# Performance work log

Measured on AMD Instinct MI355X. Metric: run time of the kernel, lower is better.

The kernel has to match this reference:

```python
import jax, jax.numpy as jnp
import numpy as np

B, S, D, H = 4, 2048, 1024, 16
HD = D // H


def setup_inputs() -> dict:
    key = jax.random.key(0)
    ks = jax.random.split(key, 11)
    s = 1.0 / np.sqrt(D)
    return {
        "query": jax.random.normal(ks[0], (B, S, D), jnp.float32),
        "key": jax.random.normal(ks[1], (B, S, D), jnp.float32),
        "value": jax.random.normal(ks[2], (B, S, D), jnp.float32),
        "Wq": jax.random.normal(ks[3], (D, D), jnp.float32) * s,
        "bq": jax.random.normal(ks[4], (D,), jnp.float32) * s,
        "Wk": jax.random.normal(ks[5], (D, D), jnp.float32) * s,
        "bk": jax.random.normal(ks[6], (D,), jnp.float32) * s,
        "Wv": jax.random.normal(ks[7], (D, D), jnp.float32) * s,
        "bv": jax.random.normal(ks[8], (D,), jnp.float32) * s,
        "Wo": jax.random.normal(ks[9], (D, D), jnp.float32) * s,
        "bo": jax.random.normal(ks[10], (D,), jnp.float32) * s,
    }


def reference(query, key, value, Wq, bq, Wk, bk, Wv, bv, Wo, bo):
    b = query.shape[0]
    # projections (torch Linear: x @ W.T + b)
    q = (query @ Wq.T + bq).reshape(b, -1, H, HD).transpose(0, 2, 1, 3)  # [B,H,S,hd]
    k = (key @ Wk.T + bk).reshape(b, -1, H, HD).transpose(0, 2, 1, 3)
    v = (value @ Wv.T + bv).reshape(b, -1, H, HD).transpose(0, 2, 1, 3)
    scores = jnp.einsum('bhqd,bhkd->bhqk', q, k) / jnp.sqrt(jnp.float32(HD))
    attn = jax.nn.softmax(scores, axis=-1)  # dropout = identity (eval)
    out = jnp.einsum('bhqk,bhkd->bhqd', attn, v)
    out = out.transpose(0, 2, 1, 3).reshape(b, -1, D)
    return out @ Wo.T + bo
```

## Files before the change

### kernel.cpp

```cpp
#include <hip/hip_runtime.h>
#include <stdint.h>

typedef __attribute__((ext_vector_type(8))) short  s16x8;
typedef __attribute__((ext_vector_type(4))) float  f32x4;
typedef __attribute__((ext_vector_type(4))) unsigned short u16x4;

__device__ __forceinline__ unsigned short f2bf(float f) {
  union { float f; uint32_t u; } x; x.f = f;
  uint32_t u = x.u;
  return (unsigned short)((u + 0x7fffu + ((u >> 16) & 1u)) >> 16);
}

__device__ __forceinline__ float fexp2(float x) {
  float r; asm("v_exp_f32 %0, %1" : "=v"(r) : "v"(x)); return r;
}
__device__ __forceinline__ uint32_t cvtpk_bf16(float lo, float hi) {
  uint32_t r; asm("v_cvt_pk_bf16_f32 %0, %1, %2" : "=v"(r) : "v"(lo), "v"(hi)); return r;
}

__device__ __forceinline__ void gload_lds16(const void* g, void* l) {
  __builtin_amdgcn_global_load_lds(
      (const __attribute__((address_space(1))) void*)g,
      (__attribute__((address_space(3))) void*)l, 16, 0, 0);
}

struct CvtJobs {
  const float* src[7];
  unsigned short* dst[7];
  int n4[7];
};
__global__ __launch_bounds__(256) void cvt_all(CvtJobs jobs) {
  const int j = blockIdx.y;
  const float* __restrict__ src = jobs.src[j];
  unsigned short* __restrict__ dst = jobs.dst[j];
  const int n4 = jobs.n4[j];
  const int stride = gridDim.x * blockDim.x;
  for (int i = blockIdx.x * blockDim.x + threadIdx.x; i < n4; i += stride) {
    f32x4 v = *(const f32x4*)(src + (size_t)i * 4);
    u16x4 o = { f2bf(v[0]), f2bf(v[1]), f2bf(v[2]), f2bf(v[3]) };
    *(u16x4*)(dst + (size_t)i * 4) = o;
  }
}

struct GemmJob {
  const unsigned short* A;
  const unsigned short* Bmat;
  const float* bias;
  unsigned short* C;
  int M, N, Nb;
  int bias_row;
  float scale;
};

__device__ __forceinline__ void gemm_core8big(const unsigned short* __restrict__ A,
                                              const unsigned short* __restrict__ Bw,
                                              int m0, int n0, int K, char* L,
                                              f32x4 (&acc)[8][4]) {
  const int tid = threadIdx.x;
  const int l = tid & 63;
  const int lr = l & 15, lc = l >> 4;
  const int w = tid >> 6;
  const int wr = w >> 2, wc = w & 3;

  const int srow = tid >> 2;
  const int sc = (tid & 3) ^ ((srow >> 1) & 3);
  const unsigned short* sA1 = A + (size_t)(m0 + srow) * K + sc * 8;
  const unsigned short* sA2 = sA1 + (size_t)128 * K;
  const unsigned short* sB1 = Bw + (size_t)(n0 + srow) * K + sc * 8;
  const unsigned short* sB2 = sB1 + (size_t)128 * K;
  char* d1 = L + (size_t)tid * 16;
  char* d2 = d1 + 8192;
  char* d3 = d1 + 16384;
  char* d4 = d1 + 24576;

#define GSTAGE(BUF, KS) { gload_lds16(sA1 + (KS), d1 + (BUF) * 32768); \
                          gload_lds16(sA2 + (KS), d2 + (BUF) * 32768); \
                          gload_lds16(sB1 + (KS), d3 + (BUF) * 32768); \
                          gload_lds16(sB2 + (KS), d4 + (BUF) * 32768); }

  const int s16 = (lc ^ ((lr >> 1) & 3)) * 16;
  int offA[8], offB[4];
#pragma unroll
  for (int i = 0; i < 8; ++i) offA[i] = (wr * 128 + i * 16 + lr) * 64 + s16;
#pragma unroll
  for (int j = 0; j < 4; ++j) offB[j] = 16384 + (wc * 64 + j * 16 + lr) * 64 + s16;

  const int nk = K >> 5;
  GSTAGE(0, 0);
  GSTAGE(1, 32);
  int cur = 0;
  for (int t = 0; t < nk; ++t) {
    if (t < nk - 1) asm volatile("s_waitcnt vmcnt(4)" ::: "memory");
    else            asm volatile("s_waitcnt vmcnt(0)" ::: "memory");
    __builtin_amdgcn_s_barrier();
    if (t < nk - 2) {
      int nb = cur + 2; if (nb >= 3) nb -= 3;
      GSTAGE(nb, (t + 2) * 32);
    }
    const char* Lb = L + cur * 32768;
    s16x8 af[8], bfr[4];
#pragma unroll
    for (int i = 0; i < 8; ++i) af[i] = *(const s16x8*)(Lb + offA[i]);
#pragma unroll
    for (int j = 0; j < 4; ++j) bfr[j] = *(const s16x8*)(Lb + offB[j]);
    __builtin_amdgcn_s_setprio(1);
#pragma unroll
    for (int i = 0; i < 8; ++i)
#pragma unroll
      for (int j = 0; j < 4; ++j)
        acc[i][j] = __builtin_amdgcn_mfma_f32_16x16x32_bf16(af[i], bfr[j], acc[i][j], 0, 0, 0);
    __builtin_amdgcn_s_setprio(0);
    ++cur; if (cur == 3) cur = 0;
  }
#undef GSTAGE
}

__global__ __launch_bounds__(512) void gemm_qkv(GemmJob j0, GemmJob j1, GemmJob j2) {
  __shared__ __align__(16) char L[98304];
  const int f = blockIdx.x;
  const int wid = (f & 7) * 48 + (f >> 3);
  const int job = wid >> 7;
  const int i = wid & 127;
  const GemmJob jb = (job == 0) ? j0 : (job == 1) ? j1 : j2;
  const int m0 = (i / jb.Nb) * 256, n0 = (i % jb.Nb) * 256;
  f32x4 acc[8][4];
#pragma unroll
  for (int i2 = 0; i2 < 8; ++i2)
#pragma unroll
    for (int j2 = 0; j2 < 4; ++j2) acc[i2][j2] = (f32x4){0.f, 0.f, 0.f, 0.f};
  gemm_core8big(jb.A, jb.Bmat, m0, n0, 1024, L, acc);
  const int tid = threadIdx.x;
  const int l = tid & 63, w = tid >> 6;
  const int lr = l & 15, lc = l >> 4;
  const int wr = w >> 2, wc = w & 3;
#pragma unroll
  for (int i2 = 0; i2 < 8; ++i2) {
    const int row0 = m0 + wr * 128 + i2 * 16 + lc * 4;
    f32x4 brow;
    if (jb.bias_row) brow = *(const f32x4*)&jb.bias[row0];
#pragma unroll
    for (int j2 = 0; j2 < 4; ++j2) {
      const int col = n0 + wc * 64 + j2 * 16 + lr;
      float bcol = jb.bias_row ? 0.f : jb.bias[col];
#pragma unroll
      for (int r = 0; r < 4; ++r) {
        float v = (acc[i2][j2][r] + (jb.bias_row ? brow[r] : bcol)) * jb.scale;
        jb.C[(size_t)(row0 + r) * jb.N + col] = f2bf(v);
      }
    }
  }
}

__global__ __launch_bounds__(512) void gemm_out(const unsigned short* __restrict__ A,
                                                const unsigned short* __restrict__ Bw,
                                                const float* __restrict__ bias,
                                                float* __restrict__ Cout,
                                                int M, int N, int K) {
  __shared__ __align__(16) char L[98304];
  const int f = blockIdx.x;
  const int wid = (f & 7) * 16 + (f >> 3);
  const int m0 = (wid >> 2) * 256, n0 = (wid & 3) * 256;
  f32x4 acc[8][4];
#pragma unroll
  for (int i = 0; i < 8; ++i)
#pragma unroll
    for (int j = 0; j < 4; ++j) acc[i][j] = (f32x4){0.f, 0.f, 0.f, 0.f};
  gemm_core8big(A, Bw, m0, n0, K, L, acc);
  const int tid = threadIdx.x;
  const int l = tid & 63, w = tid >> 6;
  const int lr = l & 15, lc = l >> 4;
  const int wr = w >> 2, wc = w & 3;
#pragma unroll
  for (int i = 0; i < 8; ++i) {
    const int row0 = m0 + wr * 128 + i * 16 + lc * 4;
#pragma unroll
    for (int j = 0; j < 4; ++j) {
      const int col = n0 + wc * 64 + j * 16 + lr;
      float bcol = bias[col];
#pragma unroll
      for (int r = 0; r < 4; ++r)
        Cout[(size_t)(row0 + r) * N + col] = acc[i][j][r] + bcol;
    }
  }
}

__global__ __launch_bounds__(512) void attn_fwd(const unsigned short* __restrict__ qb,
                                                const unsigned short* __restrict__ kb,
                                                const unsigned short* __restrict__ vtb,
                                                unsigned short* __restrict__ ob) {
  __shared__ __align__(16) unsigned short L[3 * 8192];
  const int tid = threadIdx.x;
  const int l = tid & 63, w = tid >> 6;
  const int lr = l & 15, lc = l >> 4;
  const int i0 = blockIdx.x;
  const int wid = (i0 & 7) * 128 + (i0 >> 3);
  const int qx = wid & 15;
  const int h = (wid >> 4) & 15;
  const int b = wid >> 8;
  const int q0 = qx * 128;
  const size_t qkbase = ((size_t)b * 2048) * 1024 + (size_t)h * 64;
  const size_t vtbase = (size_t)(h * 64) * 8192 + (size_t)b * 2048;

  s16x8 aq0, aq1;
  {
    const unsigned short* qp = qb + qkbase + (size_t)(q0 + w * 16 + lr) * 1024 + lc * 8;
    aq0 = *(const s16x8*)qp;
    aq1 = *(const s16x8*)(qp + 32);
  }

  float lsum = 0.f;
  f32x4 oacc[4];
#pragma unroll
  for (int nd = 0; nd < 4; ++nd) oacc[nd] = (f32x4){0.f, 0.f, 0.f, 0.f};

  const int role = w >> 2, wk = w & 3;
  const int rl = l >> 3;
  const int cs = (l & 7) ^ rl;
  const int rA = wk * 16 + rl, rB = rA + 8;
#define RHO(rr) (8 * (((rr) >> 2) & 3) + 4 * (((rr) >> 4) & 1) + ((rr) & 3) + 32 * ((rr) >> 5))
  const unsigned short* sA;
  const unsigned short* sB;
  size_t tstep;
  if (role == 0) {
    sA = kb + qkbase + (size_t)RHO(rA) * 1024 + cs * 8;
    sB = kb + qkbase + (size_t)RHO(rB) * 1024 + cs * 8;
    tstep = (size_t)64 * 1024;
  } else {
    sA = vtb + vtbase + (size_t)rA * 8192 + cs * 8;
    sB = vtb + vtbase + (size_t)rB * 8192 + cs * 8;
    tstep = 64;
  }
#undef RHO
  char* dstL = (char*)L + role * 8192 + wk * 2048 + l * 16;

#define STAGE(BUF, T) {                                              \
    gload_lds16(sA + (size_t)(T) * tstep, dstL + (BUF) * 16384);     \
    gload_lds16(sB + (size_t)(T) * tstep, dstL + (BUF) * 16384 + 1024); }

  int off0[4];
#pragma unroll
  for (int ni = 0; ni < 4; ++ni)
    off0[ni] = (ni * 16 + lr) * 128 + ((lc ^ (lr & 7)) * 16);

  STAGE(0, 0);
  STAGE(1, 1);

  int cur = 0;
  for (int t = 0; t < 32; ++t) {
    if (t < 31) asm volatile("s_waitcnt vmcnt(2)" ::: "memory");
    else        asm volatile("s_waitcnt vmcnt(0)" ::: "memory");
    __builtin_amdgcn_s_barrier();
    if (t < 30) {
      int nb = cur + 2; if (nb >= 3) nb -= 3;
      STAGE(nb, t + 2);
    }
    const char* Lb = (const char*)L + cur * 16384;

    f32x4 sf[4];
    __builtin_amdgcn_s_setprio(1);
#pragma unroll
    for (int ni = 0; ni < 4; ++ni) {
      s16x8 k0 = *(const s16x8*)(Lb + off0[ni]);
      s16x8 k1 = *(const s16x8*)(Lb + (off0[ni] ^ 64));
      f32x4 z = (f32x4){0.f, 0.f, 0.f, 0.f};
      z = __builtin_amdgcn_mfma_f32_16x16x32_bf16(k0, aq0, z, 0, 0, 0);
      z = __builtin_amdgcn_mfma_f32_16x16x32_bf16(k1, aq1, z, 0, 0, 0);
      sf[ni] = z;
    }
    __builtin_amdgcn_s_setprio(0);

    union { uint32_t u[4]; s16x8 v; } pa0u, pa1u;
#pragma unroll
    for (int ni = 0; ni < 4; ++ni) {
      float p0 = fexp2(sf[ni][0]);
      float p1 = fexp2(sf[ni][1]);
      float p2 = fexp2(sf[ni][2]);
      float p3 = fexp2(sf[ni][3]);
      lsum += (p0 + p1) + (p2 + p3);
      uint32_t w0 = cvtpk_bf16(p0, p1);
      uint32_t w1 = cvtpk_bf16(p2, p3);
      if (ni < 2) { pa0u.u[ni * 2] = w0; pa0u.u[ni * 2 + 1] = w1; }
      else        { pa1u.u[(ni - 2) * 2] = w0; pa1u.u[(ni - 2) * 2 + 1] = w1; }
    }

    __builtin_amdgcn_s_setprio(1);
#pragma unroll
    for (int nd = 0; nd < 4; ++nd) {
      s16x8 v0 = *(const s16x8*)(Lb + 8192 + off0[nd]);
      s16x8 v1 = *(const s16x8*)(Lb + 8192 + (off0[nd] ^ 64));
      oacc[nd] = __builtin_amdgcn_mfma_f32_16x16x32_bf16(pa0u.v, v0, oacc[nd], 0, 0, 0);
      oacc[nd] = __builtin_amdgcn_mfma_f32_16x16x32_bf16(pa1u.v, v1, oacc[nd], 0, 0, 0);
    }
    __builtin_amdgcn_s_setprio(0);

    ++cur; if (cur == 3) cur = 0;
  }

  lsum += __shfl_xor(lsum, 16, 64);
  lsum += __shfl_xor(lsum, 32, 64);
  float linv[4];
#pragma unroll
  for (int r = 0; r < 4; ++r) linv[r] = 1.f / __shfl(lsum, lc * 4 + r, 64);
#pragma unroll
  for (int nd = 0; nd < 4; ++nd)
#pragma unroll
    for (int r = 0; r < 4; ++r) {
      int qrow = q0 + w * 16 + lc * 4 + r;
      ob[qkbase + (size_t)qrow * 1024 + nd * 16 + lr] = f2bf(oacc[nd][r] * linv[r]);
    }
#undef STAGE
}

extern "C" void kernel_launch(void* const* d_in, const int* in_sizes, int n_in,
                              void* d_out, int out_size, void* d_ws, size_t ws_size,
                              hipStream_t stream) {
  const float* query = (const float*)d_in[0];
  const float* key_  = (const float*)d_in[1];
  const float* value = (const float*)d_in[2];
  const float* Wq = (const float*)d_in[3];
  const float* bq = (const float*)d_in[4];
  const float* Wk = (const float*)d_in[5];
  const float* bk = (const float*)d_in[6];
  const float* Wv = (const float*)d_in[7];
  const float* bv = (const float*)d_in[8];
  const float* Wo = (const float*)d_in[9];
  const float* bo = (const float*)d_in[10];

  const int MS = 4 * 2048;
  const int D = 1024;
  const size_t NX = (size_t)MS * D;
  const size_t NW = (size_t)D * D;

  const size_t need = (6 * NX + 4 * NW) * 2;
  if (ws_size < need) return;

  unsigned short* ws  = (unsigned short*)d_ws;
  unsigned short* xq  = ws;
  unsigned short* xk  = xq + NX;
  unsigned short* xv  = xk + NX;
  unsigned short* qb_ = xv + NX;
  unsigned short* kb_ = qb_ + NX;
  unsigned short* vtb = kb_ + NX;
  unsigned short* wqb = vtb + NX;
  unsigned short* wkb = wqb + NW;
  unsigned short* wvb = wkb + NW;
  unsigned short* wob = wvb + NW;
  unsigned short* attn = xq;

  CvtJobs cj;
  cj.src[0] = query; cj.dst[0] = xq;  cj.n4[0] = (int)(NX / 4);
  cj.src[1] = key_;  cj.dst[1] = xk;  cj.n4[1] = (int)(NX / 4);
  cj.src[2] = value; cj.dst[2] = xv;  cj.n4[2] = (int)(NX / 4);
  cj.src[3] = Wq;    cj.dst[3] = wqb; cj.n4[3] = (int)(NW / 4);
  cj.src[4] = Wk;    cj.dst[4] = wkb; cj.n4[4] = (int)(NW / 4);
  cj.src[5] = Wv;    cj.dst[5] = wvb; cj.n4[5] = (int)(NW / 4);
  cj.src[6] = Wo;    cj.dst[6] = wob; cj.n4[6] = (int)(NW / 4);
  cvt_all<<<dim3(1024, 7), 256, 0, stream>>>(cj);

  const float qscale = 0.18033688f;
  GemmJob jq = { xq,  wqb, bq, qb_, MS, D,  4,  0, qscale };
  GemmJob jk = { xk,  wkb, bk, kb_, MS, D,  4,  0, 1.f };
  GemmJob jv = { wvb, xv,  bv, vtb, D,  MS, 32, 1, 1.f };
  gemm_qkv<<<dim3(384), 512, 0, stream>>>(jq, jk, jv);

  attn_fwd<<<dim3(1024), 512, 0, stream>>>(qb_, kb_, vtb, attn);

  gemm_out<<<dim3(128), 512, 0, stream>>>(attn, wob, bo, (float*)d_out, MS, D, D);
}
```

Baseline: 214.3 us.

## Restructure GEMM core to K=64 double-buffered stages and compute softmax row sums via MFMA

The shared GEMM core now stages 64-wide K tiles into a two-buffer LDS layout (128KB) with an 8-way XOR swizzle. Each K tile is split into four MFMA phases, with barriers between them and the global-to-LDS loads for the next tiles placed inside the loop. This halves the number of outer iterations and is meant to overlap loading with compute, at the cost of more LDS per block and extra barriers. Separately, the attention kernel drops the per-lane VALU sum of exponentials and the shuffle reduction. It instead gets row sums from an extra pair of MFMAs against a bf16 ones vector, which sums the bf16-rounded probabilities.

```diff
diff --git a/kernel.cpp b/kernel.cpp
--- a/kernel.cpp
+++ b/kernel.cpp
@@ -23,6 +23,8 @@
       (const __attribute__((address_space(1))) void*)g,
       (__attribute__((address_space(3))) void*)l, 16, 0, 0);
 }
+
+#define PBAR() { asm volatile("" ::: "memory"); __builtin_amdgcn_s_barrier(); }
 
 struct CvtJobs {
   const float* src[7];
@@ -52,71 +54,109 @@
   float scale;
 };
 
-__device__ __forceinline__ void gemm_core8big(const unsigned short* __restrict__ A,
-                                              const unsigned short* __restrict__ Bw,
-                                              int m0, int n0, int K, char* L,
-                                              f32x4 (&acc)[8][4]) {
+__device__ __forceinline__ void gemm_core256(const unsigned short* __restrict__ A,
+                                             const unsigned short* __restrict__ Bw,
+                                             int m0, int n0, int K, char* L,
+                                             f32x4 (&acc)[8][4]) {
   const int tid = threadIdx.x;
   const int l = tid & 63;
   const int lr = l & 15, lc = l >> 4;
   const int w = tid >> 6;
   const int wr = w >> 2, wc = w & 3;
 
-  const int srow = tid >> 2;
-  const int sc = (tid & 3) ^ ((srow >> 1) & 3);
-  const unsigned short* sA1 = A + (size_t)(m0 + srow) * K + sc * 8;
-  const unsigned short* sA2 = sA1 + (size_t)128 * K;
-  const unsigned short* sB1 = Bw + (size_t)(n0 + srow) * K + sc * 8;
-  const unsigned short* sB2 = sB1 + (size_t)128 * K;
-  char* d1 = L + (size_t)tid * 16;
-  char* d2 = d1 + 8192;
-  char* d3 = d1 + 16384;
-  char* d4 = d1 + 24576;
-
-#define GSTAGE(BUF, KS) { gload_lds16(sA1 + (KS), d1 + (BUF) * 32768); \
-                          gload_lds16(sA2 + (KS), d2 + (BUF) * 32768); \
-                          gload_lds16(sB1 + (KS), d3 + (BUF) * 32768); \
-                          gload_lds16(sB2 + (KS), d4 + (BUF) * 32768); }
-
-  const int s16 = (lc ^ ((lr >> 1) & 3)) * 16;
+  const int srow = tid >> 3;
+  const int sc = (tid & 7) ^ (srow & 7);
+  const unsigned short* sa0 = A + (size_t)(m0 + srow) * K + sc * 8;
+  const unsigned short* sa1 = A + (size_t)(m0 + 128 + srow) * K + sc * 8;
+  const unsigned short* sb0 = Bw + (size_t)(n0 + srow) * K + sc * 8;
+  const unsigned short* sb1 = Bw + (size_t)(n0 + 128 + srow) * K + sc * 8;
+  const size_t rk64 = (size_t)64 * K;
+  char* dst0 = L + (size_t)tid * 16;
+
+#define STGA(BUF, H, KT) { \
+    const unsigned short* s_ = (H) ? sa1 : sa0; \
+    gload_lds16(s_ + (size_t)(KT) * 64,        dst0 + (BUF) * 65536 + (H) * 16384); \
+    gload_lds16(s_ + rk64 + (size_t)(KT) * 64, dst0 + (BUF) * 65536 + (H) * 16384 + 8192); }
+#define STGB(BUF, H, KT) { \
+    const unsigned short* s_ = (H) ? sb1 : sb0; \
+    gload_lds16(s_ + (size_t)(KT) * 64,        dst0 + (BUF) * 65536 + 32768 + (H) * 16384); \
+    gload_lds16(s_ + rk64 + (size_t)(KT) * 64, dst0 + (BUF) * 65536 + 32768 + (H) * 16384 + 8192); }
+
+  const int c0 = ((lc) ^ (lr & 7)) << 4;
+  const int c1 = ((4 + lc) ^ (lr & 7)) << 4;
   int offA[8], offB[4];
 #pragma unroll
-  for (int i = 0; i < 8; ++i) offA[i] = (wr * 128 + i * 16 + lr) * 64 + s16;
-#pragma unroll
-  for (int j = 0; j < 4; ++j) offB[j] = 16384 + (wc * 64 + j * 16 + lr) * 64 + s16;
-
-  const int nk = K >> 5;
-  GSTAGE(0, 0);
-  GSTAGE(1, 32);
-  int cur = 0;
+  for (int i = 0; i < 8; ++i) offA[i] = (wr * 128 + i * 16 + lr) * 128;
+#pragma unroll
+  for (int j = 0; j < 4; ++j) offB[j] = 32768 + (wc * 64 + j * 16 + lr) * 128;
+
+  const int nk = K >> 6;
+  STGA(0, 0, 0); STGA(0, 1, 0); STGB(0, 0, 0); STGB(0, 1, 0);
+  STGA(1, 0, 1); STGA(1, 1, 1);
+  asm volatile("s_waitcnt vmcnt(4)" ::: "memory");
+  __builtin_amdgcn_s_barrier();
+
   for (int t = 0; t < nk; ++t) {
-    if (t < nk - 1) asm volatile("s_waitcnt vmcnt(4)" ::: "memory");
+    const int buf = t & 1;
+    const char* Lb = L + buf * 65536;
+    s16x8 a0[8], b0[4], a1[8], b1[4];
+
+    if (t + 1 < nk) STGB(buf ^ 1, 0, t + 1);
+#pragma unroll
+    for (int i = 0; i < 8; ++i) a0[i] = *(const s16x8*)(Lb + offA[i] + c0);
+#pragma unroll
+    for (int j = 0; j < 4; ++j) b0[j] = *(const s16x8*)(Lb + offB[j] + c0);
+    __builtin_amdgcn_s_setprio(1);
+#pragma unroll
+    for (int i = 0; i < 8; ++i) {
+      acc[i][0] = __builtin_amdgcn_mfma_f32_16x16x32_bf16(a0[i], b0[0], acc[i][0], 0, 0, 0);
+      acc[i][1] = __builtin_amdgcn_mfma_f32_16x16x32_bf16(a0[i], b0[1], acc[i][1], 0, 0, 0);
+    }
+    __builtin_amdgcn_s_setprio(0);
+    PBAR();
+
+    if (t + 1 < nk) STGB(buf ^ 1, 1, t + 1);
+    __builtin_amdgcn_s_setprio(1);
+#pragma unroll
+    for (int i = 0; i < 8; ++i) {
+      acc[i][2] = __builtin_amdgcn_mfma_f32_16x16x32_bf16(a0[i], b0[2], acc[i][2], 0, 0, 0);
+      acc[i][3] = __builtin_amdgcn_mfma_f32_16x16x32_bf16(a0[i], b0[3], acc[i][3], 0, 0, 0);
+    }
+    __builtin_amdgcn_s_setprio(0);
+    PBAR();
+
+#pragma unroll
+    for (int i = 0; i < 8; ++i) a1[i] = *(const s16x8*)(Lb + offA[i] + c1);
+#pragma unroll
+    for (int j = 0; j < 4; ++j) b1[j] = *(const s16x8*)(Lb + offB[j] + c1);
+    __builtin_amdgcn_s_setprio(1);
+#pragma unroll
+    for (int i = 0; i < 8; ++i) {
+      acc[i][0] = __builtin_amdgcn_mfma_f32_16x16x32_bf16(a1[i], b1[0], acc[i][0], 0, 0, 0);
+      acc[i][1] = __builtin_amdgcn_mfma_f32_16x16x32_bf16(a1[i], b1[1], acc[i][1], 0, 0, 0);
+    }
+    __builtin_amdgcn_s_setprio(0);
+    asm volatile("s_waitcnt lgkmcnt(0)" ::: "memory");
+    __builtin_amdgcn_s_barrier();
+
+    if (t + 2 < nk) { STGA(buf, 0, t + 2); STGA(buf, 1, t + 2); }
+    __builtin_amdgcn_s_setprio(1);
+#pragma unroll
+    for (int i = 0; i < 8; ++i) {
+      acc[i][2] = __builtin_amdgcn_mfma_f32_16x16x32_bf16(a1[i], b1[2], acc[i][2], 0, 0, 0);
+      acc[i][3] = __builtin_amdgcn_mfma_f32_16x16x32_bf16(a1[i], b1[3], acc[i][3], 0, 0, 0);
+    }
+    __builtin_amdgcn_s_setprio(0);
+    if (t + 2 < nk) asm volatile("s_waitcnt vmcnt(4)" ::: "memory");
     else            asm volatile("s_waitcnt vmcnt(0)" ::: "memory");
     __builtin_amdgcn_s_barrier();
-    if (t < nk - 2) {
-      int nb = cur + 2; if (nb >= 3) nb -= 3;
-      GSTAGE(nb, (t + 2) * 32);
-    }
-    const char* Lb = L + cur * 32768;
-    s16x8 af[8], bfr[4];
-#pragma unroll
-    for (int i = 0; i < 8; ++i) af[i] = *(const s16x8*)(Lb + offA[i]);
-#pragma unroll
-    for (int j = 0; j < 4; ++j) bfr[j] = *(const s16x8*)(Lb + offB[j]);
-    __builtin_amdgcn_s_setprio(1);
-#pragma unroll
-    for (int i = 0; i < 8; ++i)
-#pragma unroll
-      for (int j = 0; j < 4; ++j)
-        acc[i][j] = __builtin_amdgcn_mfma_f32_16x16x32_bf16(af[i], bfr[j], acc[i][j], 0, 0, 0);
-    __builtin_amdgcn_s_setprio(0);
-    ++cur; if (cur == 3) cur = 0;
-  }
-#undef GSTAGE
+  }
+#undef STGA
+#undef STGB
 }
 
 __global__ __launch_bounds__(512) void gemm_qkv(GemmJob j0, GemmJob j1, GemmJob j2) {
-  __shared__ __align__(16) char L[98304];
+  __shared__ __align__(16) char L[131072];
   const int f = blockIdx.x;
   const int wid = (f & 7) * 48 + (f >> 3);
   const int job = wid >> 7;
@@ -128,7 +168,7 @@
   for (int i2 = 0; i2 < 8; ++i2)
 #pragma unroll
     for (int j2 = 0; j2 < 4; ++j2) acc[i2][j2] = (f32x4){0.f, 0.f, 0.f, 0.f};
-  gemm_core8big(jb.A, jb.Bmat, m0, n0, 1024, L, acc);
+  gemm_core256(jb.A, jb.Bmat, m0, n0, 1024, L, acc);
   const int tid = threadIdx.x;
   const int l = tid & 63, w = tid >> 6;
   const int lr = l & 15, lc = l >> 4;
@@ -156,7 +196,7 @@
                                                 const float* __restrict__ bias,
                                                 float* __restrict__ Cout,
                                                 int M, int N, int K) {
-  __shared__ __align__(16) char L[98304];
+  __shared__ __align__(16) char L[131072];
   const int f = blockIdx.x;
   const int wid = (f & 7) * 16 + (f >> 3);
   const int m0 = (wid >> 2) * 256, n0 = (wid & 3) * 256;
@@ -165,7 +205,7 @@
   for (int i = 0; i < 8; ++i)
 #pragma unroll
     for (int j = 0; j < 4; ++j) acc[i][j] = (f32x4){0.f, 0.f, 0.f, 0.f};
-  gemm_core8big(A, Bw, m0, n0, K, L, acc);
+  gemm_core256(A, Bw, m0, n0, K, L, acc);
   const int tid = threadIdx.x;
   const int l = tid & 63, w = tid >> 6;
   const int lr = l & 15, lc = l >> 4;
@@ -208,8 +248,13 @@
     aq1 = *(const s16x8*)(qp + 32);
   }
 
-  float lsum = 0.f;
+  union { u16x4 h4[2]; s16x8 v; } onesu;
+#pragma unroll
+  for (int i = 0; i < 2; ++i) onesu.h4[i] = (u16x4){0x3F80, 0x3F80, 0x3F80, 0x3F80};
+  const s16x8 bones = onesu.v;
+
   f32x4 oacc[4];
+  f32x4 oextra = (f32x4){0.f, 0.f, 0.f, 0.f};
 #pragma unroll
   for (int nd = 0; nd < 4; ++nd) oacc[nd] = (f32x4){0.f, 0.f, 0.f, 0.f};
 
@@ -276,7 +321,6 @@
       float p1 = fexp2(sf[ni][1]);
       float p2 = fexp2(sf[ni][2]);
       float p3 = fexp2(sf[ni][3]);
-      lsum += (p0 + p1) + (p2 + p3);
       uint32_t w0 = cvtpk_bf16(p0, p1);
       uint32_t w1 = cvtpk_bf16(p2, p3);
       if (ni < 2) { pa0u.u[ni * 2] = w0; pa0u.u[ni * 2 + 1] = w1; }
@@ -291,16 +335,16 @@
       oacc[nd] = __builtin_amdgcn_mfma_f32_16x16x32_bf16(pa0u.v, v0, oacc[nd], 0, 0, 0);
       oacc[nd] = __builtin_amdgcn_mfma_f32_16x16x32_bf16(pa1u.v, v1, oacc[nd], 0, 0, 0);
     }
+    oextra = __builtin_amdgcn_mfma_f32_16x16x32_bf16(pa0u.v, bones, oextra, 0, 0, 0);
+    oextra = __builtin_amdgcn_mfma_f32_16x16x32_bf16(pa1u.v, bones, oextra, 0, 0, 0);
     __builtin_amdgcn_s_setprio(0);
 
     ++cur; if (cur == 3) cur = 0;
   }
 
-  lsum += __shfl_xor(lsum, 16, 64);
-  lsum += __shfl_xor(lsum, 32, 64);
   float linv[4];
 #pragma unroll
-  for (int r = 0; r < 4; ++r) linv[r] = 1.f / __shfl(lsum, lc * 4 + r, 64);
+  for (int r = 0; r < 4; ++r) linv[r] = 1.f / oextra[r];
 #pragma unroll
   for (int nd = 0; nd < 4; ++nd)
 #pragma unroll
```

Measured after the change: 208.3 us. 2.8% less time.
